# Optimization experiments

Measured on AMD Instinct MI355X. Metric: run time of the kernel, lower is better.

## Reference

```python
import jax, jax.numpy as jnp
import numpy as np
import math

B, S, DIM = 2, 2048, 4096
N_HEADS, N_KV = 32, 8
HD = DIM // N_HEADS           # 128
N_REP = N_HEADS // N_KV       # 4
MAX_SEQ = 2048


def _rope_freqs(seq_len, head_dim):
    inv = 1.0 / (10000.0 ** (np.arange(0, head_dim, 2, dtype=np.float32) / head_dim))
    ang = np.outer(np.arange(seq_len, dtype=np.float32), inv)  # [S, HD/2]
    return jnp.asarray(np.cos(ang)), jnp.asarray(np.sin(ang))


def setup_inputs() -> dict:
    key = jax.random.key(0)
    ks = jax.random.split(key, 5)
    x = jax.random.normal(ks[0], (B, S, DIM), dtype=jnp.float32)
    wq = jax.random.normal(ks[1], (DIM, N_HEADS * HD), dtype=jnp.float32) * 0.02
    wk = jax.random.normal(ks[2], (DIM, N_KV * HD), dtype=jnp.float32) * 0.02
    wv = jax.random.normal(ks[3], (DIM, N_KV * HD), dtype=jnp.float32) * 0.02
    wo = jax.random.normal(ks[4], (N_HEADS * HD, DIM), dtype=jnp.float32) * 0.02
    freqs_cos, freqs_sin = _rope_freqs(S, HD)
    return {"x": x, "wq": wq, "wk": wk, "wv": wv, "wo": wo,
            "freqs_cos": freqs_cos, "freqs_sin": freqs_sin, "start_pos": 0}


def _apply_rope(t, cos, sin):
    # t: [B, S, H, HD]; adjacent pairs (2i, 2i+1) form complex numbers
    tr = t.reshape(*t.shape[:-1], HD // 2, 2)
    xr, xi = tr[..., 0], tr[..., 1]
    c = cos[None, :, None, :]  # [1, S, 1, HD/2]
    s = sin[None, :, None, :]
    o = jnp.stack([xr * c - xi * s, xr * s + xi * c], axis=-1)
    return o.reshape(t.shape)


def reference(x, wq, wk, wv, wo, freqs_cos, freqs_sin, start_pos):
    batch, seq_len, _ = x.shape
    q = (x @ wq).reshape(batch, seq_len, N_HEADS, HD)
    k = (x @ wk).reshape(batch, seq_len, N_KV, HD)
    v = (x @ wv).reshape(batch, seq_len, N_KV, HD)
    xq = _apply_rope(q, freqs_cos, freqs_sin)
    xk = _apply_rope(k, freqs_cos, freqs_sin)

    # KV-cache append (buffer initialized to zeros, as in the module)
    cache_k = jnp.zeros((batch, MAX_SEQ, N_KV, HD), dtype=x.dtype)
    cache_v = jnp.zeros((batch, MAX_SEQ, N_KV, HD), dtype=x.dtype)
    cache_k = jax.lax.dynamic_update_slice(cache_k, xk, (0, start_pos, 0, 0))
    cache_v = jax.lax.dynamic_update_slice(cache_v, v, (0, start_pos, 0, 0))
    keys = cache_k[:, : start_pos + seq_len]    # [B, T, KV, HD]
    values = cache_v[:, : start_pos + seq_len]

    # GQA: repeat kv heads n_rep times
    keys = jnp.repeat(keys, N_REP, axis=2)      # [B, T, H, HD]
    values = jnp.repeat(values, N_REP, axis=2)

    # [B, H, Sq, T] scores; no causal mask, matching the original module
    scores = jnp.einsum("bqhd,bkhd->bhqk", xq, keys) / math.sqrt(HD)
    attn = jax.nn.softmax(scores, axis=-1)
    out = jnp.einsum("bhqk,bkhd->bqhd", attn, values)
    out = out.reshape(batch, seq_len, N_HEADS * HD)
    return out @ wo
```

## Files before the change

### kernel.cpp

```cpp
#include <hip/hip_runtime.h>

#define S_LEN 2048

typedef __bf16 bf16x8 __attribute__((ext_vector_type(8)));
typedef float f32x4 __attribute__((ext_vector_type(4)));

static __device__ __forceinline__ unsigned short f32_to_bf16(float f){
  unsigned int u = __float_as_uint(f);
  u += 0x7FFFu + ((u >> 16) & 1u);
  return (unsigned short)(u >> 16);
}
static __device__ __forceinline__ float bf16_to_f32(unsigned short h){
  return __uint_as_float(((unsigned int)h) << 16);
}
static __device__ __forceinline__ bf16x8 ld_bf16x8(const unsigned short* p){
  return *reinterpret_cast<const bf16x8*>(p);
}
static __device__ __forceinline__ void async_copy16(const void* g, void* l){
  __builtin_amdgcn_global_load_lds(
      (const __attribute__((address_space(1))) void*)g,
      (__attribute__((address_space(3))) void*)l, 16, 0, 0);
}

__global__ void conv_f32_bf16(const float* __restrict__ in, unsigned short* __restrict__ out, int n4){
  int i = blockIdx.x * 256 + threadIdx.x;
  if (i >= n4) return;
  float4 v = ((const float4*)in)[i];
  ushort4 o;
  o.x = f32_to_bf16(v.x); o.y = f32_to_bf16(v.y);
  o.z = f32_to_bf16(v.z); o.w = f32_to_bf16(v.w);
  ((ushort4*)out)[i] = o;
}

__global__ void transpose_w(const float* __restrict__ in, unsigned short* __restrict__ out, int K, int N){
  __shared__ float tile[32][33];
  int n0 = blockIdx.x * 32, k0 = blockIdx.y * 32;
  int tx = threadIdx.x, ty = threadIdx.y;
  #pragma unroll
  for (int i=0;i<4;++i)
    tile[ty + i*8][tx] = in[(size_t)(k0 + ty + i*8) * N + n0 + tx];
  __syncthreads();
  #pragma unroll
  for (int i=0;i<4;++i)
    out[(size_t)(n0 + ty + i*8) * K + k0 + tx] = f32_to_bf16(tile[tx][ty + i*8]);
}

__global__ void transpose_v(const unsigned short* __restrict__ in, unsigned short* __restrict__ out){
  __shared__ unsigned short tile[32][33];
  int r0 = blockIdx.x * 32;
  int c0 = blockIdx.y * 32;
  int tx = threadIdx.x, ty = threadIdx.y;
  #pragma unroll
  for (int i=0;i<4;++i)
    tile[ty + i*8][tx] = in[(size_t)(r0 + ty + i*8) * 6144 + 5120 + c0 + tx];
  __syncthreads();
  #pragma unroll
  for (int i=0;i<4;++i)
    out[(size_t)(c0 + ty + i*8) * 4096 + r0 + tx] = tile[tx][ty + i*8];
}

__global__ void rope_inplace(unsigned short* __restrict__ t, const float* __restrict__ cs,
                             const float* __restrict__ sn, int heads, float scale){
  int idx = blockIdx.x * 256 + threadIdx.x;
  int j = idx & 63;
  int tmp = idx >> 6;
  int h = tmp & (heads - 1);
  int row = tmp / heads;
  int s = row & (S_LEN - 1);
  float c = cs[s*64 + j], si = sn[s*64 + j];
  size_t base = (size_t)row * 6144 + (h << 7) + (j << 1);
  float xr = bf16_to_f32(t[base]);
  float xi = bf16_to_f32(t[base + 1]);
  t[base]     = f32_to_bf16((xr * c - xi * si) * scale);
  t[base + 1] = f32_to_bf16((xr * si + xi * c) * scale);
}

template<bool OUT_BF16>
__global__ __launch_bounds__(256, 2) void gemm_bt(
    const unsigned short* __restrict__ A,
    const unsigned short* __restrict__ Bt,
    void* __restrict__ Cout, int N, int K)
{
  __shared__ alignas(16) unsigned short Asm[128 * 32];
  __shared__ alignas(16) unsigned short Bsm[128 * 32];
  const int tid  = threadIdx.x;
  const int wave = tid >> 6;
  const int lane = tid & 63;
  const int lm = lane & 15;
  const int kq = lane >> 4;
  const int wm = (wave >> 1) * 64;
  const int wn = (wave & 1) * 64;
  const size_t bm = (size_t)blockIdx.y * 128;
  const size_t bn = (size_t)blockIdx.x * 128;

  const f32x4 zero4 = {0.f, 0.f, 0.f, 0.f};
  f32x4 acc[4][4];
  #pragma unroll
  for (int i=0;i<4;++i)
    #pragma unroll
    for (int j=0;j<4;++j) acc[i][j] = zero4;

  const int srow = lane >> 2;
  const int sc   = ((lane & 3) ^ ((lane >> 3) & 3)) * 8;
  const unsigned short* gA0 = A  + (bm + wave*32      + srow) * (size_t)K + sc;
  const unsigned short* gA1 = A  + (bm + wave*32 + 16 + srow) * (size_t)K + sc;
  const unsigned short* gB0 = Bt + (bn + wave*32      + srow) * (size_t)K + sc;
  const unsigned short* gB1 = Bt + (bn + wave*32 + 16 + srow) * (size_t)K + sc;
  unsigned short* lA0 = &Asm[(wave*32     ) * 32];
  unsigned short* lA1 = &Asm[(wave*32 + 16) * 32];
  unsigned short* lB0 = &Bsm[(wave*32     ) * 32];
  unsigned short* lB1 = &Bsm[(wave*32 + 16) * 32];

  const int p8 = (kq ^ ((lm >> 1) & 3)) * 8;

  for (int k0 = 0; k0 < K; k0 += 32){
    async_copy16(gA0, lA0);
    async_copy16(gA1, lA1);
    async_copy16(gB0, lB0);
    async_copy16(gB1, lB1);
    gA0 += 32; gA1 += 32; gB0 += 32; gB1 += 32;
    __syncthreads();

    bf16x8 af[4], bfr[4];
    #pragma unroll
    for (int i=0;i<4;++i){
      af[i]  = ld_bf16x8(&Asm[(wm + i*16 + lm)*32 + p8]);
      bfr[i] = ld_bf16x8(&Bsm[(wn + i*16 + lm)*32 + p8]);
    }
    #pragma unroll
    for (int mi=0; mi<4; ++mi)
      #pragma unroll
      for (int ni=0; ni<4; ++ni)
        acc[mi][ni] = __builtin_amdgcn_mfma_f32_16x16x32_bf16(af[mi], bfr[ni], acc[mi][ni], 0, 0, 0);
    __syncthreads();
  }

  #pragma unroll
  for (int mi=0; mi<4; ++mi){
    #pragma unroll
    for (int ni=0; ni<4; ++ni){
      #pragma unroll
      for (int r=0; r<4; ++r){
        size_t row = bm + wm + mi*16 + kq*4 + r;
        size_t col = bn + wn + ni*16 + lm;
        if constexpr (OUT_BF16)
          ((unsigned short*)Cout)[row * N + col] = f32_to_bf16(acc[mi][ni][r]);
        else
          ((float*)Cout)[row * N + col] = acc[mi][ni][r];
      }
    }
  }
}

#define PP 72
#define QKV_STRIDE 6144

__global__ __launch_bounds__(256, 2) void flash_attn(
    const unsigned short* __restrict__ QKV,
    const unsigned short* __restrict__ VT,
    unsigned short* __restrict__ O)
{
  __shared__ alignas(16) unsigned short Ksm[64 * 128];
  __shared__ alignas(16) unsigned short VTsm[128 * 64];
  __shared__ alignas(16) unsigned short Psm[4 * 32 * PP];

  const int tid  = threadIdx.x;
  const int wave = tid >> 6;
  const int lane = tid & 63;
  const int lm = lane & 15;
  const int kq = lane >> 4;
  const int b   = blockIdx.z;
  const int h   = blockIdx.y;
  const int kvh = h >> 2;
  const int q0  = blockIdx.x * 128;

  bf16x8 qf[2][4];
  #pragma unroll
  for (int mt=0; mt<2; ++mt){
    const size_t qbase = (size_t)(b * S_LEN + q0 + mt*64 + wave*16 + lm) * QKV_STRIDE + h * 128;
    #pragma unroll
    for (int kf=0; kf<4; ++kf)
      qf[mt][kf] = ld_bf16x8(&QKV[qbase + kf*32 + kq*8]);
  }

  const f32x4 zero4 = {0.f,0.f,0.f,0.f};
  f32x4 Oacc[2][8];
  #pragma unroll
  for (int mt=0; mt<2; ++mt)
    #pragma unroll
    for (int i=0;i<8;++i) Oacc[mt][i] = zero4;
  f32x4 lacc[2] = {zero4, zero4};

  union { unsigned short s[8]; bf16x8 v; } ou;
  #pragma unroll
  for (int i=0;i<8;++i) ou.s[i] = 0x3F80;
  const bf16x8 ones = ou.v;

  const unsigned short* Kg = QKV + 4096 + (size_t)kvh * 128 + (size_t)b * S_LEN * QKV_STRIDE;
  const unsigned short* Vg = VT + (size_t)kvh * 128 * 4096 + (size_t)b * S_LEN;
  unsigned short* Pw = &Psm[wave * 32 * PP];

  const int kkey_in = lane >> 4;
  const int kccp    = lane & 15;
  const int vd_in   = lane >> 3;
  const int vchl    = ((lane & 7) ^ (vd_in & 7)) * 8;

  for (int kt = 0; kt < S_LEN/64; ++kt){
    #pragma unroll
    for (int c=0;c<4;++c){
      int kb4 = (wave*4 + c) * 4;
      int key = kb4 + kkey_in;
      int ccl = kccp ^ (key & 7);
      async_copy16(Kg + (size_t)(kt*64 + key) * QKV_STRIDE + ccl*8, &Ksm[kb4 * 128]);
    }
    #pragma unroll
    for (int c=0;c<4;++c){
      int d0 = (wave*4 + c) * 8;
      int d  = d0 + vd_in;
      async_copy16(Vg + (size_t)d * 4096 + kt*64 + vchl, &VTsm[d0 * 64]);
    }
    __syncthreads();

    f32x4 sacc[2][4];
    #pragma unroll
    for (int nt=0;nt<4;++nt){ sacc[0][nt] = zero4; sacc[1][nt] = zero4; }
    #pragma unroll
    for (int nt=0; nt<4; ++nt){
      const int n = nt*16 + lm;
      #pragma unroll
      for (int kf=0; kf<4; ++kf){
        int pc = ((kf*4 + kq) ^ (lm & 7)) * 8;
        bf16x8 kfrag = ld_bf16x8(&Ksm[n*128 + pc]);
        sacc[0][nt] = __builtin_amdgcn_mfma_f32_16x16x32_bf16(qf[0][kf], kfrag, sacc[0][nt], 0,0,0);
        sacc[1][nt] = __builtin_amdgcn_mfma_f32_16x16x32_bf16(qf[1][kf], kfrag, sacc[1][nt], 0,0,0);
      }
    }

    #pragma unroll
    for (int mt=0; mt<2; ++mt){
      #pragma unroll
      for (int nt=0; nt<4; ++nt){
        #pragma unroll
        for (int e=0; e<4; ++e){
          float p = __expf(sacc[mt][nt][e]);
          Pw[(mt*16 + kq*4 + e)*PP + nt*16 + lm] = f32_to_bf16(p);
        }
      }
    }

    #pragma unroll
    for (int kf2=0; kf2<2; ++kf2){
      bf16x8 pf0 = ld_bf16x8(&Pw[(     lm)*PP + kf2*32 + kq*8]);
      bf16x8 pf1 = ld_bf16x8(&Pw[(16 + lm)*PP + kf2*32 + kq*8]);
      lacc[0] = __builtin_amdgcn_mfma_f32_16x16x32_bf16(pf0, ones, lacc[0], 0,0,0);
      lacc[1] = __builtin_amdgcn_mfma_f32_16x16x32_bf16(pf1, ones, lacc[1], 0,0,0);
      #pragma unroll
      for (int dt=0; dt<8; ++dt){
        int pc = ((kf2*4 + kq) ^ (lm & 7)) * 8;
        bf16x8 vfr = ld_bf16x8(&VTsm[(dt*16 + lm)*64 + pc]);
        Oacc[0][dt] = __builtin_amdgcn_mfma_f32_16x16x32_bf16(pf0, vfr, Oacc[0][dt], 0,0,0);
        Oacc[1][dt] = __builtin_amdgcn_mfma_f32_16x16x32_bf16(pf1, vfr, Oacc[1][dt], 0,0,0);
      }
    }
    __syncthreads();
  }

  #pragma unroll
  for (int mt=0; mt<2; ++mt){
    float inv[4];
    #pragma unroll
    for (int r=0;r<4;++r) inv[r] = __builtin_amdgcn_rcpf(lacc[mt][r]);
    const size_t obase = (((size_t)(b * S_LEN + q0 + mt*64 + wave*16 + kq*4)) * 32 + h) * 128;
    #pragma unroll
    for (int r=0;r<4;++r){
      #pragma unroll
      for (int dt=0; dt<8; ++dt)
        O[obase + (size_t)r * 4096 + dt*16 + lm] = f32_to_bf16(Oacc[mt][dt][r] * inv[r]);
    }
  }
}

extern "C" void kernel_launch(void* const* d_in, const int* in_sizes, int n_in,
                              void* d_out, int out_size, void* d_ws, size_t ws_size,
                              hipStream_t stream)
{
  const float* x    = (const float*)d_in[0];
  const float* wq   = (const float*)d_in[1];
  const float* wk   = (const float*)d_in[2];
  const float* wv   = (const float*)d_in[3];
  const float* wo   = (const float*)d_in[4];
  const float* fcos = (const float*)d_in[5];
  const float* fsin = (const float*)d_in[6];

  float* out = (float*)d_out;
  char* w = (char*)d_ws;
  const size_t MB = 1ull << 20;
  unsigned short* xb    = (unsigned short*)(w + 0);
  unsigned short* wqkvT = (unsigned short*)(w + 32*MB);
  unsigned short* woT   = (unsigned short*)(w + 80*MB);
  unsigned short* qkv   = (unsigned short*)(w + 112*MB);
  unsigned short* vT    = (unsigned short*)(w + 32*MB);
  unsigned short* attn  = (unsigned short*)(w + 0);

  conv_f32_bf16<<<dim3(16384), dim3(256), 0, stream>>>(x, xb, 4194304);

  transpose_w<<<dim3(128,128), dim3(32,8), 0, stream>>>(wq, wqkvT,                      4096, 4096);
  transpose_w<<<dim3(32,128),  dim3(32,8), 0, stream>>>(wk, wqkvT + (size_t)4096*4096, 4096, 1024);
  transpose_w<<<dim3(32,128),  dim3(32,8), 0, stream>>>(wv, wqkvT + (size_t)5120*4096, 4096, 1024);
  transpose_w<<<dim3(128,128), dim3(32,8), 0, stream>>>(wo, woT, 4096, 4096);

  gemm_bt<true><<<dim3(48,32), dim3(256), 0, stream>>>(xb, wqkvT, qkv, 6144, 4096);

  rope_inplace<<<dim3(32768), dim3(256), 0, stream>>>(qkv,        fcos, fsin, 32, 0.08838834764831845f);
  rope_inplace<<<dim3(8192),  dim3(256), 0, stream>>>(qkv + 4096, fcos, fsin, 8, 1.0f);

  transpose_v<<<dim3(128,32), dim3(32,8), 0, stream>>>(qkv, vT);

  flash_attn<<<dim3(16, 32, 2), dim3(256), 0, stream>>>(qkv, vT, attn);

  gemm_bt<false><<<dim3(32,32), dim3(256), 0, stream>>>(attn, woT, out, 4096, 4096);
}
```

Baseline: 831.6 us.

## Replace GEMM with 256x256-tile double-buffered async-copy pipelined kernel

Swaps the 128x128, single-buffered, sync-heavy GEMM for a 256x256-tile kernel with 8 waves, a K step of 64 and two LDS buffers (128 KB). Global-to-LDS async copies for the next tiles are interleaved with the MFMA quads, with explicit vmcnt/lgkmcnt waits, barriers and setprio. The aim is to hide memory latency and raise data reuse in both the QKV and output projections. In exchange it uses the full LDS and heavy register pressure, which may limit occupancy. Launching 384 and 256 blocks may also leave CUs unevenly loaded.

After: 737.7 us. 11.3% less time.

```diff
diff --git a/kernel.cpp b/kernel.cpp
--- a/kernel.cpp
+++ b/kernel.cpp
@@ -75,78 +75,145 @@
   t[base + 1] = f32_to_bf16((xr * si + xi * c) * scale);
 }
 
+#define MFMA16 __builtin_amdgcn_mfma_f32_16x16x32_bf16
+#define GBAR()   asm volatile("s_barrier" ::: "memory")
+#define LGKM0()  do { asm volatile("s_waitcnt lgkmcnt(0)" ::: "memory"); \
+                      __builtin_amdgcn_sched_barrier(0); } while(0)
+#define VMW(N)   asm volatile("s_waitcnt vmcnt(" #N ")" ::: "memory")
+#define STG(gp, lp) do { \
+    async_copy16((gp),             (lp) + wofs); \
+    async_copy16((gp) + (Ks<<6),   (lp) + 4096 + wofs); \
+  } while(0)
+
+static __device__ __forceinline__ void read_a4(bf16x8 (&a)[4][2], const unsigned short* base, int s0, int s1){
+  #pragma unroll
+  for (int m=0;m<4;++m){
+    const unsigned short* p = base + m*1024;
+    a[m][0] = ld_bf16x8(p + s0);
+    a[m][1] = ld_bf16x8(p + s1);
+  }
+}
+template<int NO>
+static __device__ __forceinline__ void read_b2(bf16x8 (&b)[4][2], const unsigned short* base, int s0, int s1){
+  #pragma unroll
+  for (int n=0;n<2;++n){
+    const unsigned short* p = base + (NO+n)*1024;
+    b[NO+n][0] = ld_bf16x8(p + s0);
+    b[NO+n][1] = ld_bf16x8(p + s1);
+  }
+}
+template<int MO, int NO>
+static __device__ __forceinline__ void mfma_quad(f32x4 (&acc)[8][4], const bf16x8 (&a)[4][2], const bf16x8 (&b)[4][2]){
+  __builtin_amdgcn_s_setprio(1);
+  #pragma unroll
+  for (int ks=0; ks<2; ++ks)
+    #pragma unroll
+    for (int m=0;m<4;++m)
+      #pragma unroll
+      for (int n=0;n<2;++n)
+        acc[MO+m][NO+n] = MFMA16(a[m][ks], b[NO+n][ks], acc[MO+m][NO+n], 0, 0, 0);
+  __builtin_amdgcn_s_setprio(0);
+}
+
 template<bool OUT_BF16>
-__global__ __launch_bounds__(256, 2) void gemm_bt(
+__global__ __launch_bounds__(512, 2) void gemm256_bt(
     const unsigned short* __restrict__ A,
     const unsigned short* __restrict__ Bt,
     void* __restrict__ Cout, int N, int K)
 {
-  __shared__ alignas(16) unsigned short Asm[128 * 32];
-  __shared__ alignas(16) unsigned short Bsm[128 * 32];
+  __shared__ alignas(16) unsigned short sm[65536];
+  unsigned short* A0 = sm;
+  unsigned short* B0 = sm + 16384;
+  unsigned short* A1 = sm + 32768;
+  unsigned short* B1 = sm + 49152;
+
   const int tid  = threadIdx.x;
   const int wave = tid >> 6;
   const int lane = tid & 63;
   const int lm = lane & 15;
   const int kq = lane >> 4;
-  const int wm = (wave >> 1) * 64;
-  const int wn = (wave & 1) * 64;
-  const size_t bm = (size_t)blockIdx.y * 128;
-  const size_t bn = (size_t)blockIdx.x * 128;
-
-  const f32x4 zero4 = {0.f, 0.f, 0.f, 0.f};
-  f32x4 acc[4][4];
-  #pragma unroll
-  for (int i=0;i<4;++i)
+  const int wm = wave >> 2;
+  const int wn = wave & 3;
+  const int wofs = wave * 512;
+  const int srow = wave * 8 + (lane >> 3);
+  const int scol = ((lane & 7) ^ (lane >> 3)) * 8;
+  const int s0 = (kq ^ (lm & 7)) * 8;
+  const int s1 = s0 ^ 32;
+
+  const size_t Ks = (size_t)K;
+  const size_t bm = (size_t)blockIdx.y * 256;
+  const size_t bn = (size_t)blockIdx.x * 256;
+  const unsigned short* Asrc = A  + (bm + srow) * Ks + scol;
+  const unsigned short* Bsrc = Bt + (bn + srow) * Ks + scol;
+  const size_t h1 = (size_t)128 * Ks;
+
+  const int ardo = (wm*128 + lm) * 64;
+  const int brdo = (wn*64  + lm) * 64;
+
+  const f32x4 zero4 = {0.f,0.f,0.f,0.f};
+  f32x4 acc[8][4];
+  #pragma unroll
+  for (int i=0;i<8;++i)
     #pragma unroll
     for (int j=0;j<4;++j) acc[i][j] = zero4;
-
-  const int srow = lane >> 2;
-  const int sc   = ((lane & 3) ^ ((lane >> 3) & 3)) * 8;
-  const unsigned short* gA0 = A  + (bm + wave*32      + srow) * (size_t)K + sc;
-  const unsigned short* gA1 = A  + (bm + wave*32 + 16 + srow) * (size_t)K + sc;
-  const unsigned short* gB0 = Bt + (bn + wave*32      + srow) * (size_t)K + sc;
-  const unsigned short* gB1 = Bt + (bn + wave*32 + 16 + srow) * (size_t)K + sc;
-  unsigned short* lA0 = &Asm[(wave*32     ) * 32];
-  unsigned short* lA1 = &Asm[(wave*32 + 16) * 32];
-  unsigned short* lB0 = &Bsm[(wave*32     ) * 32];
-  unsigned short* lB1 = &Bsm[(wave*32 + 16) * 32];
-
-  const int p8 = (kq ^ ((lm >> 1) & 3)) * 8;
-
-  for (int k0 = 0; k0 < K; k0 += 32){
-    async_copy16(gA0, lA0);
-    async_copy16(gA1, lA1);
-    async_copy16(gB0, lB0);
-    async_copy16(gB1, lB1);
-    gA0 += 32; gA1 += 32; gB0 += 32; gB1 += 32;
-    __syncthreads();
-
-    bf16x8 af[4], bfr[4];
-    #pragma unroll
-    for (int i=0;i<4;++i){
-      af[i]  = ld_bf16x8(&Asm[(wm + i*16 + lm)*32 + p8]);
-      bfr[i] = ld_bf16x8(&Bsm[(wn + i*16 + lm)*32 + p8]);
-    }
-    #pragma unroll
-    for (int mi=0; mi<4; ++mi)
-      #pragma unroll
-      for (int ni=0; ni<4; ++ni)
-        acc[mi][ni] = __builtin_amdgcn_mfma_f32_16x16x32_bf16(af[mi], bfr[ni], acc[mi][ni], 0, 0, 0);
-    __syncthreads();
-  }
-
-  #pragma unroll
-  for (int mi=0; mi<4; ++mi){
+  bf16x8 a[4][2], b[4][2];
+
+  const int NT = K >> 6;
+
+  STG(Bsrc,           B0);
+  STG(Bsrc + h1,      B0 + 8192);
+  STG(Asrc,           A0);
+  STG(Asrc + h1,      A0 + 8192);
+  STG(Bsrc + 64,      B1);
+  STG(Bsrc + h1 + 64, B1 + 8192);
+  VMW(4);
+  GBAR();
+
+  for (int it = 0; it < (NT >> 1); ++it){
+    const int k1 = (2*it + 1) * 64;
+    const int k2 = ((2*it + 2) & (NT - 1)) * 64;
+    const int k3 = ((2*it + 3) & (NT - 1)) * 64;
+    read_a4(a, A0 + ardo, s0, s1);
+    read_b2<0>(b, B0 + brdo, s0, s1);
+    STG(Asrc + k1, A1);
+    GBAR(); LGKM0(); mfma_quad<0,0>(acc, a, b); GBAR();
+    read_b2<2>(b, B0 + brdo, s0, s1);
+    STG(Asrc + h1 + k1, A1 + 8192);
+    GBAR(); LGKM0(); mfma_quad<0,2>(acc, a, b); GBAR();
+    read_a4(a, A0 + ardo + 4096, s0, s1);
+    STG(Bsrc + k2, B0);
+    GBAR(); LGKM0(); mfma_quad<4,0>(acc, a, b); GBAR();
+    STG(Bsrc + h1 + k2, B0 + 8192);
+    VMW(4);
+    GBAR(); LGKM0(); mfma_quad<4,2>(acc, a, b); GBAR();
+    read_a4(a, A1 + ardo, s0, s1);
+    read_b2<0>(b, B1 + brdo, s0, s1);
+    STG(Asrc + k2, A0);
+    GBAR(); LGKM0(); mfma_quad<0,0>(acc, a, b); GBAR();
+    read_b2<2>(b, B1 + brdo, s0, s1);
+    STG(Asrc + h1 + k2, A0 + 8192);
+    GBAR(); LGKM0(); mfma_quad<0,2>(acc, a, b); GBAR();
+    read_a4(a, A1 + ardo + 4096, s0, s1);
+    STG(Bsrc + k3, B1);
+    GBAR(); LGKM0(); mfma_quad<4,0>(acc, a, b); GBAR();
+    STG(Bsrc + h1 + k3, B1 + 8192);
+    VMW(4);
+    GBAR(); LGKM0(); mfma_quad<4,2>(acc, a, b); GBAR();
+  }
+  VMW(0);
+
+  #pragma unroll
+  for (int mi=0; mi<8; ++mi){
+    const size_t row = bm + wm*128 + mi*16 + kq*4;
     #pragma unroll
     for (int ni=0; ni<4; ++ni){
+      const size_t col = bn + wn*64 + ni*16 + lm;
       #pragma unroll
       for (int r=0; r<4; ++r){
-        size_t row = bm + wm + mi*16 + kq*4 + r;
-        size_t col = bn + wn + ni*16 + lm;
         if constexpr (OUT_BF16)
-          ((unsigned short*)Cout)[row * N + col] = f32_to_bf16(acc[mi][ni][r]);
+          ((unsigned short*)Cout)[(row + r) * N + col] = f32_to_bf16(acc[mi][ni][r]);
         else
-          ((float*)Cout)[row * N + col] = acc[mi][ni][r];
+          ((float*)Cout)[(row + r) * N + col] = acc[mi][ni][r];
       }
     }
   }
@@ -309,7 +376,7 @@
   transpose_w<<<dim3(32,128),  dim3(32,8), 0, stream>>>(wv, wqkvT + (size_t)5120*4096, 4096, 1024);
   transpose_w<<<dim3(128,128), dim3(32,8), 0, stream>>>(wo, woT, 4096, 4096);
 
-  gemm_bt<true><<<dim3(48,32), dim3(256), 0, stream>>>(xb, wqkvT, qkv, 6144, 4096);
+  gemm256_bt<true><<<dim3(24,16), dim3(512), 0, stream>>>(xb, wqkvT, qkv, 6144, 4096);
 
   rope_inplace<<<dim3(32768), dim3(256), 0, stream>>>(qkv,        fcos, fsin, 32, 0.08838834764831845f);
   rope_inplace<<<dim3(8192),  dim3(256), 0, stream>>>(qkv + 4096, fcos, fsin, 8, 1.0f);
@@ -318,5 +385,5 @@
 
   flash_attn<<<dim3(16, 32, 2), dim3(256), 0, stream>>>(qkv, vT, attn);
 
-  gemm_bt<false><<<dim3(32,32), dim3(256), 0, stream>>>(attn, woT, out, 4096, 4096);
-}
+  gemm256_bt<false><<<dim3(16,16), dim3(512), 0, stream>>>(attn, woT, out, 4096, 4096);
+}
```
